# Optimization experiments

Hardware: AMD Instinct MI355X
Metric: run time of the kernel (lower is better)

Reference implementation:

```python
import jax, jax.numpy as jnp
import numpy as np

D = 512      # d_model
H = 8        # num_heads
HD = D // H  # head_dim = 64
NI = 3       # num_inputs


def setup_inputs() -> dict:
    key = jax.random.key(0)
    ks = jax.random.split(key, 20)
    b, n, ni = 4, 8192, 4096
    s = 0.02
    inp = {
        "x": jax.random.normal(ks[0], (b, n, D), jnp.float32),
        "emb0": jax.random.normal(ks[1], (b, ni, D), jnp.float32),
        "emb1": jax.random.normal(ks[2], (b, ni, D), jnp.float32),
        "emb2": jax.random.normal(ks[3], (b, ni, D), jnp.float32),
        "Wq": jax.random.normal(ks[4], (D, D), jnp.float32) * s,
        "bq": jnp.zeros((D,), jnp.float32),
        "Wk": jax.random.normal(ks[5], (NI, D, D), jnp.float32) * s,
        "bk": jnp.zeros((NI, D), jnp.float32),
        "Wv": jax.random.normal(ks[6], (NI, D, D), jnp.float32) * s,
        "bv": jnp.zeros((NI, D), jnp.float32),
        "Wo": jax.random.normal(ks[7], (D, D), jnp.float32) * s,
        "bo": jnp.zeros((D,), jnp.float32),
        "mask0": jax.random.randint(ks[8], (b, ni), 0, 2).astype(bool),
        "mask1": jax.random.randint(ks[9], (b, ni), 0, 2).astype(bool),
        "mask2": jax.random.randint(ks[10], (b, ni), 0, 2).astype(bool),
    }
    return inp


def _heads(t, b):
    # [b, n, D] -> [b, H, n, HD]
    return t.reshape(b, -1, H, HD).transpose(0, 2, 1, 3)


def reference(x, emb0, emb1, emb2, Wq, bq, Wk, bk, Wv, bv, Wo, bo, mask0, mask1, mask2):
    b, n, _ = x.shape
    q = jax.nn.softmax(_heads(x @ Wq.T + bq, b), axis=-1)  # [b,H,n,HD]
    out = q
    for i, (emb, mask) in enumerate(((emb0, mask0), (emb1, mask1), (emb2, mask2))):
        k = jax.nn.softmax(_heads(emb @ Wk[i].T + bk[i], b), axis=-1)  # [b,H,ni,HD]
        v = _heads(emb @ Wv[i].T + bv[i], b)                            # [b,H,ni,HD]
        k = jnp.where(mask[:, None, :, None], k, 0.0)
        k_sum = k.sum(axis=2, keepdims=True)                            # [b,H,1,HD]
        d_inv = 1.0 / jnp.sum(q * k_sum, axis=-1, keepdims=True)        # [b,H,n,1]
        kv = jnp.einsum('bhsd,bhse->bhde', k, v)                        # [b,H,HD,HD]
        out = out + jnp.einsum('bhnd,bhde->bhne', q, kv) * d_inv
    out = out.transpose(0, 2, 1, 3).reshape(b, n, D) / NI
    return out @ Wo.T + bo
```

## Files before the change

kernel.cpp:

```cpp
#include <hip/hip_runtime.h>

#define D_MODEL 512
#define NH 8
#define HD_ 64
#define NUM_I 3
#define B_ 4
#define NSEQ 8192
#define SSEQ 4096

typedef __attribute__((ext_vector_type(8))) short short8;
typedef __attribute__((ext_vector_type(4))) float floatx4;

static constexpr size_t Q_OFF    = 0;
static constexpr size_t KBUF_OFF = 8388608;
static constexpr size_t VBUF_OFF = 16777216;
static constexpr size_t EMBB_OFF = 25165824;
static constexpr size_t WB_OFF   = 29360128;
static constexpr size_t KV_OFF   = 30408704;
static constexpr size_t KS_OFF   = 30801920;
static constexpr size_t FLAG_OFF = 30808064;

__device__ __forceinline__ float bf2f(unsigned short u) {
    union { unsigned i; float f; } v; v.i = ((unsigned)u) << 16; return v.f;
}
__device__ __forceinline__ unsigned short f2bf(float f) {
    union { float f; unsigned i; } v; v.f = f;
    unsigned r = v.i + 0x7fffu + ((v.i >> 16) & 1u);
    return (unsigned short)(r >> 16);
}

__device__ __forceinline__ void gld16(const void* g, void* l) {
    __builtin_amdgcn_global_load_lds((const __attribute__((address_space(1))) void*)g,
                                     (__attribute__((address_space(3))) void*)l, 16, 0, 0);
}

__global__ void mask_mode_kernel(const int* __restrict__ m, int* __restrict__ flag)
{
    __shared__ int any;
    if (threadIdx.x == 0) any = 0;
    __syncthreads();
    const unsigned v = (unsigned)m[threadIdx.x];
    if (v > 1u) atomicOr(&any, 1);
    __syncthreads();
    if (threadIdx.x == 0) *flag = any;
}

__global__ __launch_bounds__(256)
void f2bf_kernel(const float* __restrict__ in, unsigned short* __restrict__ out, int n8)
{
    const int i = blockIdx.x * 256 + threadIdx.x;
    if (i >= n8) return;
    const float4 a = ((const float4*)in)[2*i];
    const float4 b = ((const float4*)in)[2*i + 1];
    short8 r;
    r[0] = (short)f2bf(a.x); r[1] = (short)f2bf(a.y);
    r[2] = (short)f2bf(a.z); r[3] = (short)f2bf(a.w);
    r[4] = (short)f2bf(b.x); r[5] = (short)f2bf(b.y);
    r[6] = (short)f2bf(b.z); r[7] = (short)f2bf(b.w);
    ((short8*)out)[i] = r;
}

template<int EPI, bool BF16OUT>
__global__ __launch_bounds__(256)
void proj_mfma(const unsigned short* __restrict__ A, const unsigned short* __restrict__ W,
               const float* __restrict__ bias, const int* __restrict__ mask,
               const int* __restrict__ maskmode, void* __restrict__ Cv)
{
    __shared__ short As[4096];
    __shared__ short Bs[4096];
    const int tid  = threadIdx.x;
    const int wid  = tid >> 6, lane = tid & 63;
    const int wm   = wid & 1,  wn   = wid >> 1;
    const int l15  = lane & 15, lq  = lane >> 4;
    const int m0   = blockIdx.x * 128;
    const int n0   = blockIdx.y * 128;

    floatx4 acc[4][4] = {};

    const int srow = tid & 127;
    const int sks  = tid >> 7;
    const unsigned short* Ag = A + (size_t)(m0 + srow) * D_MODEL + sks * 8;
    const unsigned short* Wg = W + (size_t)(n0 + srow) * D_MODEL + sks * 8;
    short* AsW = As + wid * 512;
    short* BsW = Bs + wid * 512;

    const int aoff = (lq * 128 + wm * 64 + l15) * 8;
    const int boff = (lq * 128 + wn * 64 + l15) * 8;

    for (int k0 = 0; k0 < D_MODEL; k0 += 32) {
        __syncthreads();
        gld16(Ag + k0,      AsW);
        gld16(Ag + k0 + 16, AsW + 2048);
        gld16(Wg + k0,      BsW);
        gld16(Wg + k0 + 16, BsW + 2048);
        __syncthreads();
        short8 af[4], bfv[4];
#pragma unroll
        for (int mt = 0; mt < 4; ++mt) af[mt]  = *(const short8*)&As[aoff + mt * 128];
#pragma unroll
        for (int nt = 0; nt < 4; ++nt) bfv[nt] = *(const short8*)&Bs[boff + nt * 128];
#pragma unroll
        for (int mt = 0; mt < 4; ++mt)
#pragma unroll
            for (int nt = 0; nt < 4; ++nt)
                acc[mt][nt] = __builtin_amdgcn_mfma_f32_16x16x32_bf16(af[mt], bfv[nt], acc[mt][nt], 0, 0, 0);
    }

    float bl[4];
#pragma unroll
    for (int nt = 0; nt < 4; ++nt) bl[nt] = bias[n0 + wn * 64 + nt * 16 + l15];
#pragma unroll
    for (int mt = 0; mt < 4; ++mt)
#pragma unroll
        for (int nt = 0; nt < 4; ++nt)
#pragma unroll
            for (int r = 0; r < 4; ++r) acc[mt][nt][r] += bl[nt];

    if (EPI >= 1) {
#pragma unroll
        for (int mt = 0; mt < 4; ++mt)
#pragma unroll
            for (int r = 0; r < 4; ++r) {
                float mx = fmaxf(fmaxf(acc[mt][0][r], acc[mt][1][r]),
                                 fmaxf(acc[mt][2][r], acc[mt][3][r]));
#pragma unroll
                for (int off = 1; off < 16; off <<= 1) mx = fmaxf(mx, __shfl_xor(mx, off));
                float s = 0.f;
#pragma unroll
                for (int nt = 0; nt < 4; ++nt) {
                    const float e = __expf(acc[mt][nt][r] - mx);
                    acc[mt][nt][r] = e; s += e;
                }
#pragma unroll
                for (int off = 1; off < 16; off <<= 1) s += __shfl_xor(s, off);
                const float inv = 1.f / s;
#pragma unroll
                for (int nt = 0; nt < 4; ++nt) acc[mt][nt][r] *= inv;
            }
    }
    if (EPI == 2) {
        const int bytemode = *maskmode;
#pragma unroll
        for (int mt = 0; mt < 4; ++mt)
#pragma unroll
            for (int r = 0; r < 4; ++r) {
                const int grow = m0 + wm * 64 + mt * 16 + lq * 4 + r;
                const bool keep = bytemode ? (((const unsigned char*)mask)[grow] != 0)
                                           : (mask[grow] != 0);
                if (!keep) {
#pragma unroll
                    for (int nt = 0; nt < 4; ++nt) acc[mt][nt][r] = 0.f;
                }
            }
    }

#pragma unroll
    for (int mt = 0; mt < 4; ++mt)
#pragma unroll
        for (int r = 0; r < 4; ++r) {
            const size_t row = m0 + wm * 64 + mt * 16 + lq * 4 + r;
#pragma unroll
            for (int nt = 0; nt < 4; ++nt) {
                const int col = n0 + wn * 64 + nt * 16 + l15;
                if (BF16OUT)
                    ((unsigned short*)Cv)[row * D_MODEL + col] = f2bf(acc[mt][nt][r]);
                else
                    ((float*)Cv)[row * D_MODEL + col] = acc[mt][nt][r];
            }
        }
}

__global__ __launch_bounds__(256)
void kv_accum_kernel(const float* __restrict__ K, const float* __restrict__ V,
                     float* __restrict__ kv, float* __restrict__ ksum, int i_idx)
{
    const int chunk = blockIdx.x;
    const int h = blockIdx.y;
    const int b = blockIdx.z;
    __shared__ __align__(16) float ks[32][68];
    __shared__ __align__(16) float vs[32][68];
    const int tid = threadIdx.x;
    const int tx = tid & 15, ty = tid >> 4;
    const int lrow = tid >> 4;
    const int lq = (tid & 15) << 2;
    float acc[4][4];
#pragma unroll
    for (int r = 0; r < 4; ++r)
#pragma unroll
        for (int c = 0; c < 4; ++c) acc[r][c] = 0.f;
    float ksloc = 0.f;
    const size_t base = (size_t)b * SSEQ * D_MODEL + h * HD_;

    for (int s0 = chunk*512; s0 < chunk*512 + 512; s0 += 32) {
        const float4 k0v = *(const float4*)&K[base + (size_t)(s0+lrow)    * D_MODEL + lq];
        const float4 k1v = *(const float4*)&K[base + (size_t)(s0+lrow+16) * D_MODEL + lq];
        const float4 v0v = *(const float4*)&V[base + (size_t)(s0+lrow)    * D_MODEL + lq];
        const float4 v1v = *(const float4*)&V[base + (size_t)(s0+lrow+16) * D_MODEL + lq];
        __syncthreads();
        *(float4*)&ks[lrow][lq]    = k0v;
        *(float4*)&ks[lrow+16][lq] = k1v;
        *(float4*)&vs[lrow][lq]    = v0v;
        *(float4*)&vs[lrow+16][lq] = v1v;
        __syncthreads();
#pragma unroll
        for (int s = 0; s < 32; ++s) {
            const float4 ka = *(const float4*)&ks[s][ty*4];
            const float4 vb = *(const float4*)&vs[s][tx*4];
            const float av[4] = {ka.x,ka.y,ka.z,ka.w};
            const float bv[4] = {vb.x,vb.y,vb.z,vb.w};
#pragma unroll
            for (int r = 0; r < 4; ++r)
#pragma unroll
                for (int c = 0; c < 4; ++c)
                    acc[r][c] = fmaf(av[r], bv[c], acc[r][c]);
        }
        if (tid < 64) {
#pragma unroll
            for (int s = 0; s < 32; ++s) ksloc += ks[s][tid];
        }
    }
    float* kvb = kv + ((size_t)((i_idx*B_ + b)*NH + h) << 12);
#pragma unroll
    for (int r = 0; r < 4; ++r)
#pragma unroll
        for (int c = 0; c < 4; ++c)
            atomicAdd(&kvb[(ty*4+r)*HD_ + tx*4+c], acc[r][c]);
    if (tid < 64)
        atomicAdd(&ksum[(size_t)((i_idx*B_ + b)*NH + h)*HD_ + tid], ksloc);
}

__global__ __launch_bounds__(256)
void combine_kernel(const unsigned short* __restrict__ Q, const float* __restrict__ kv,
                    const float* __restrict__ ksum, unsigned short* __restrict__ Qo)
{
    const int m0 = blockIdx.x * 128;
    const int h  = blockIdx.y;
    const int b  = m0 >> 13;
    __shared__ __align__(16) float Qt[64][128];
    __shared__ __align__(16) float Bs[64][68];
    __shared__ float sk[NUM_I][64];
    __shared__ float dinv[NUM_I][128];
    const int tid = threadIdx.x;
    const int tx = tid & 15, ty = tid >> 4;

#pragma unroll
    for (int it = 0; it < 4; ++it) {
        const int j = tid + it*256;
        const int row = j >> 3;
        const int c0  = (j & 7) << 3;
        const short8 g = *(const short8*)&Q[(size_t)(m0+row)*D_MODEL + h*HD_ + c0];
#pragma unroll
        for (int t = 0; t < 8; ++t) Qt[c0+t][row] = bf2f((unsigned short)g[t]);
    }
    if (tid < NUM_I*64) {
        const int i = tid >> 6, d = tid & 63;
        sk[i][d] = ksum[(size_t)((i*B_ + b)*NH + h)*HD_ + d];
    }
    __syncthreads();
    for (int idx = tid; idx < NUM_I*128; idx += 256) {
        const int i = idx >> 7, row = idx & 127;
        float dsum = 0.f;
#pragma unroll
        for (int dd = 0; dd < 64; ++dd) dsum += Qt[dd][row] * sk[i][dd];
        dinv[i][row] = 1.f / dsum;
    }

    float accO[8][4];
#pragma unroll
    for (int r = 0; r < 8; ++r)
#pragma unroll
        for (int c = 0; c < 4; ++c) accO[r][c] = 0.f;

    for (int i = 0; i < NUM_I; ++i) {
        const float* kvb = kv + ((size_t)((i*B_ + b)*NH + h) << 12);
        __syncthreads();
#pragma unroll
        for (int it = 0; it < 4; ++it) {
            const int j = tid + it*256;
            *(float4*)&Bs[j >> 4][(j & 15) << 2] = *(const float4*)&kvb[(size_t)j << 2];
        }
        __syncthreads();
        float part[8][4];
#pragma unroll
        for (int r = 0; r < 8; ++r)
#pragma unroll
            for (int c = 0; c < 4; ++c) part[r][c] = 0.f;
#pragma unroll
        for (int kk = 0; kk < 64; ++kk) {
            const float4 fa0 = *(const float4*)&Qt[kk][ty*8];
            const float4 fa1 = *(const float4*)&Qt[kk][ty*8+4];
            const float4 fb  = *(const float4*)&Bs[kk][tx*4];
            const float av[8] = {fa0.x,fa0.y,fa0.z,fa0.w,fa1.x,fa1.y,fa1.z,fa1.w};
            const float bv[4] = {fb.x,fb.y,fb.z,fb.w};
#pragma unroll
            for (int r = 0; r < 8; ++r)
#pragma unroll
                for (int c = 0; c < 4; ++c)
                    part[r][c] = fmaf(av[r], bv[c], part[r][c]);
        }
#pragma unroll
        for (int r = 0; r < 8; ++r) {
            const float dv = dinv[i][ty*8 + r];
#pragma unroll
            for (int c = 0; c < 4; ++c) accO[r][c] = fmaf(part[r][c], dv, accO[r][c]);
        }
    }
    const float inv3 = 1.f / 3.f;
#pragma unroll
    for (int r = 0; r < 8; ++r) {
        const int row = ty*8 + r;
        ushort4 o;
        o.x = f2bf((Qt[tx*4+0][row] + accO[r][0]) * inv3);
        o.y = f2bf((Qt[tx*4+1][row] + accO[r][1]) * inv3);
        o.z = f2bf((Qt[tx*4+2][row] + accO[r][2]) * inv3);
        o.w = f2bf((Qt[tx*4+3][row] + accO[r][3]) * inv3);
        *(ushort4*)&Qo[(size_t)(m0+row)*D_MODEL + h*HD_ + tx*4] = o;
    }
}

extern "C" void kernel_launch(void* const* d_in, const int* in_sizes, int n_in,
                              void* d_out, int out_size, void* d_ws, size_t ws_size,
                              hipStream_t stream)
{
    const float* x      = (const float*)d_in[0];
    const float* emb[3] = {(const float*)d_in[1], (const float*)d_in[2], (const float*)d_in[3]};
    const float* Wq = (const float*)d_in[4];
    const float* bq = (const float*)d_in[5];
    const float* Wk = (const float*)d_in[6];
    const float* bk = (const float*)d_in[7];
    const float* Wv = (const float*)d_in[8];
    const float* bv = (const float*)d_in[9];
    const float* Wo = (const float*)d_in[10];
    const float* bo = (const float*)d_in[11];
    const int* mask[3] = {(const int*)d_in[12], (const int*)d_in[13], (const int*)d_in[14]};
    float* out = (float*)d_out;

    float* ws = (float*)d_ws;
    unsigned short* qb   = (unsigned short*)(ws + Q_OFF);
    float*          kbuf = ws + KBUF_OFF;
    float*          vbuf = ws + VBUF_OFF;
    unsigned short* xb   = (unsigned short*)(ws + VBUF_OFF);
    unsigned short* embb = (unsigned short*)(ws + EMBB_OFF);
    unsigned short* wb   = (unsigned short*)(ws + WB_OFF);
    unsigned short* wqb  = wb;
    unsigned short* wkb  = wb + 262144;
    unsigned short* wvb  = wb + 1048576;
    unsigned short* wob  = wb + 1835008;
    unsigned short* q2b  = (unsigned short*)(ws + KBUF_OFF);
    float* kv   = ws + KV_OFF;
    float* ksum = ws + KS_OFF;
    int*   flag = (int*)(ws + FLAG_OFF);

    mask_mode_kernel<<<1, 256, 0, stream>>>(mask[0], flag);
    hipMemsetAsync(kv, 0, (size_t)(NUM_I*B_*NH*HD_*HD_ + NUM_I*B_*NH*HD_) * sizeof(float), stream);

    f2bf_kernel<<<8192, 256, 0, stream>>>(x,  xb,  2097152);
    f2bf_kernel<<<128,  256, 0, stream>>>(Wq, wqb, 32768);
    f2bf_kernel<<<384,  256, 0, stream>>>(Wk, wkb, 98304);
    f2bf_kernel<<<384,  256, 0, stream>>>(Wv, wvb, 98304);
    f2bf_kernel<<<128,  256, 0, stream>>>(Wo, wob, 32768);

    const dim3 gq(B_*NSEQ/128, D_MODEL/128);
    const dim3 gk(B_*SSEQ/128, D_MODEL/128);

    proj_mfma<1, true ><<<gq, 256, 0, stream>>>(xb, wqb, bq, nullptr, nullptr, qb);
    for (int i = 0; i < NUM_I; ++i) {
        f2bf_kernel<<<4096, 256, 0, stream>>>(emb[i], embb, 1048576);
        proj_mfma<2, false><<<gk, 256, 0, stream>>>(embb, wkb + (size_t)i*262144,
                                                    bk + (size_t)i*D_MODEL, mask[i], flag, kbuf);
        proj_mfma<0, false><<<gk, 256, 0, stream>>>(embb, wvb + (size_t)i*262144,
                                                    bv + (size_t)i*D_MODEL, nullptr, nullptr, vbuf);
        kv_accum_kernel<<<dim3(8, NH, B_), 256, 0, stream>>>(kbuf, vbuf, kv, ksum, i);
    }
    combine_kernel<<<dim3(B_*NSEQ/128, NH), 256, 0, stream>>>(qb, kv, ksum, q2b);
    proj_mfma<0, false><<<gq, 256, 0, stream>>>(q2b, wob, bo, nullptr, nullptr, out);
}
```

Baseline: 712.8 us.

## Move KV accumulation and combine to bf16 MFMA with transposed K/V layout

The K and V projections now write bf16 outputs transposed per head (head-dim rows by sequence), staged through shared memory. This lets a new MFMA-based kv-accumulation kernel read contiguous sequence chunks and compute the key sum with a ones-vector MFMA. The combine step also uses MFMA, reading a bf16 copy of the kv state. This removes the fp32 scalar FMA loops and halves K/V intermediate traffic. The cost is extra bf16 rounding of K, V and kv, plus a small conversion kernel.

```diff
diff --git a/kernel.cpp b/kernel.cpp
--- a/kernel.cpp
+++ b/kernel.cpp
@@ -12,13 +12,16 @@
 typedef __attribute__((ext_vector_type(4))) float floatx4;
 
 static constexpr size_t Q_OFF    = 0;
-static constexpr size_t KBUF_OFF = 8388608;
-static constexpr size_t VBUF_OFF = 16777216;
-static constexpr size_t EMBB_OFF = 25165824;
-static constexpr size_t WB_OFF   = 29360128;
-static constexpr size_t KV_OFF   = 30408704;
-static constexpr size_t KS_OFF   = 30801920;
-static constexpr size_t FLAG_OFF = 30808064;
+static constexpr size_t KT_OFF   = 8388608;
+static constexpr size_t VT_OFF   = 12582912;
+static constexpr size_t XB_OFF   = 8388608;
+static constexpr size_t Q2_OFF   = 8388608;
+static constexpr size_t EMBB_OFF = 16777216;
+static constexpr size_t WB_OFF   = 20971520;
+static constexpr size_t KV_OFF   = 22020096;
+static constexpr size_t KS_OFF   = 22413312;
+static constexpr size_t KVB_OFF  = 22419456;
+static constexpr size_t FLAG_OFF = 22616064;
 
 __device__ __forceinline__ float bf2f(unsigned short u) {
     union { unsigned i; float f; } v; v.i = ((unsigned)u) << 16; return v.f;
@@ -28,7 +31,6 @@
     unsigned r = v.i + 0x7fffu + ((v.i >> 16) & 1u);
     return (unsigned short)(r >> 16);
 }
-
 __device__ __forceinline__ void gld16(const void* g, void* l) {
     __builtin_amdgcn_global_load_lds((const __attribute__((address_space(1))) void*)g,
                                      (__attribute__((address_space(3))) void*)l, 16, 0, 0);
@@ -60,14 +62,15 @@
     ((short8*)out)[i] = r;
 }
 
-template<int EPI, bool BF16OUT>
+template<int EPI, int OUT>
 __global__ __launch_bounds__(256)
 void proj_mfma(const unsigned short* __restrict__ A, const unsigned short* __restrict__ W,
                const float* __restrict__ bias, const int* __restrict__ mask,
                const int* __restrict__ maskmode, void* __restrict__ Cv)
 {
-    __shared__ short As[4096];
-    __shared__ short Bs[4096];
+    __shared__ short smem[(OUT == 2) ? 18432 : 8192];
+    short* As = smem;
+    short* Bs = smem + 4096;
     const int tid  = threadIdx.x;
     const int wid  = tid >> 6, lane = tid & 63;
     const int wm   = wid & 1,  wn   = wid >> 1;
@@ -154,168 +157,193 @@
             }
     }
 
-#pragma unroll
-    for (int mt = 0; mt < 4; ++mt)
-#pragma unroll
-        for (int r = 0; r < 4; ++r) {
-            const size_t row = m0 + wm * 64 + mt * 16 + lq * 4 + r;
+    if (OUT == 2) {
+        __syncthreads();
+        short* tw = smem + wid * 4608;
+#pragma unroll
+        for (int mt = 0; mt < 4; ++mt)
 #pragma unroll
             for (int nt = 0; nt < 4; ++nt) {
-                const int col = n0 + wn * 64 + nt * 16 + l15;
-                if (BF16OUT)
-                    ((unsigned short*)Cv)[row * D_MODEL + col] = f2bf(acc[mt][nt][r]);
-                else
-                    ((float*)Cv)[row * D_MODEL + col] = acc[mt][nt][r];
-            }
+                ushort4 p;
+                p.x = f2bf(acc[mt][nt][0]); p.y = f2bf(acc[mt][nt][1]);
+                p.z = f2bf(acc[mt][nt][2]); p.w = f2bf(acc[mt][nt][3]);
+                *(ushort4*)&tw[(nt*16 + l15)*72 + mt*16 + lq*4] = p;
+            }
+        __syncthreads();
+        const int b_idx = m0 >> 12;
+        const int s_base = (m0 & 4095) + wm * 64;
+        const int h = (n0 >> 6) + wn;
+        unsigned short* outp = (unsigned short*)Cv +
+            ((size_t)(b_idx * NH + h) * 64 + lane) * SSEQ + s_base;
+        const short* src = &tw[lane * 72];
+#pragma unroll
+        for (int sc = 0; sc < 8; ++sc)
+            *(short8*)&outp[sc*8] = *(const short8*)&src[sc*8];
+    } else {
+#pragma unroll
+        for (int mt = 0; mt < 4; ++mt)
+#pragma unroll
+            for (int r = 0; r < 4; ++r) {
+                const size_t row = m0 + wm * 64 + mt * 16 + lq * 4 + r;
+#pragma unroll
+                for (int nt = 0; nt < 4; ++nt) {
+                    const int col = n0 + wn * 64 + nt * 16 + l15;
+                    if (OUT == 1)
+                        ((unsigned short*)Cv)[row * D_MODEL + col] = f2bf(acc[mt][nt][r]);
+                    else
+                        ((float*)Cv)[row * D_MODEL + col] = acc[mt][nt][r];
+                }
+            }
+    }
+}
+
+__global__ __launch_bounds__(256)
+void kv_accum_mfma(const unsigned short* __restrict__ kT, const unsigned short* __restrict__ vT,
+                   float* __restrict__ kv, float* __restrict__ ksum, int i_idx)
+{
+    const int chunk = blockIdx.x;
+    const int h = blockIdx.y, b = blockIdx.z;
+    __shared__ short As[2048];
+    __shared__ short Bs[2048];
+    const int tid = threadIdx.x;
+    const int wid = tid >> 6, lane = tid & 63;
+    const int wm  = wid & 1,  wn  = wid >> 1;
+    const int l15 = lane & 15, lq = lane >> 4;
+
+    const size_t base = (size_t)(b * NH + h) * 64 * SSEQ + chunk * 512;
+    const int srow = tid & 63, ssub = tid >> 6;
+    const unsigned short* Ag = vT + base + (size_t)srow * SSEQ + ssub * 8;
+    const unsigned short* Bg = kT + base + (size_t)srow * SSEQ + ssub * 8;
+    short* AsW = As + wid * 512;
+    short* BsW = Bs + wid * 512;
+
+    floatx4 acc[2][2] = {};
+    floatx4 ks[2] = {};
+    short8 ones;
+#pragma unroll
+    for (int j = 0; j < 8; ++j) ones[j] = (short)0x3F80;
+
+    const int aoff = (wm*32 + l15)*8;
+    const int boff = (wn*32 + l15)*8;
+
+    for (int k0 = 0; k0 < 512; k0 += 32) {
+        __syncthreads();
+        gld16(Ag + k0, AsW);
+        gld16(Bg + k0, BsW);
+        __syncthreads();
+        short8 af[2], bfr[2];
+#pragma unroll
+        for (int mt = 0; mt < 2; ++mt) af[mt]  = *(const short8*)&As[lq*512 + aoff + mt*128];
+#pragma unroll
+        for (int nt = 0; nt < 2; ++nt) bfr[nt] = *(const short8*)&Bs[lq*512 + boff + nt*128];
+#pragma unroll
+        for (int mt = 0; mt < 2; ++mt)
+#pragma unroll
+            for (int nt = 0; nt < 2; ++nt)
+                acc[mt][nt] = __builtin_amdgcn_mfma_f32_16x16x32_bf16(af[mt], bfr[nt], acc[mt][nt], 0, 0, 0);
+        if (wm == 0) {
+#pragma unroll
+            for (int nt = 0; nt < 2; ++nt)
+                ks[nt] = __builtin_amdgcn_mfma_f32_16x16x32_bf16(ones, bfr[nt], ks[nt], 0, 0, 0);
         }
+    }
+    float* kvb = kv + (size_t)((i_idx*B_ + b)*NH + h) * 4096;
+#pragma unroll
+    for (int mt = 0; mt < 2; ++mt)
+#pragma unroll
+        for (int nt = 0; nt < 2; ++nt)
+#pragma unroll
+            for (int r = 0; r < 4; ++r) {
+                const int e = wm*32 + mt*16 + lq*4 + r;
+                const int d = wn*32 + nt*16 + l15;
+                atomicAdd(&kvb[e*64 + d], acc[mt][nt][r]);
+            }
+    if (wm == 0 && lq == 0) {
+        float* ksb = ksum + (size_t)((i_idx*B_ + b)*NH + h) * 64;
+#pragma unroll
+        for (int nt = 0; nt < 2; ++nt)
+            atomicAdd(&ksb[wn*32 + nt*16 + l15], ks[nt][0]);
+    }
 }
 
 __global__ __launch_bounds__(256)
-void kv_accum_kernel(const float* __restrict__ K, const float* __restrict__ V,
-                     float* __restrict__ kv, float* __restrict__ ksum, int i_idx)
-{
-    const int chunk = blockIdx.x;
-    const int h = blockIdx.y;
-    const int b = blockIdx.z;
-    __shared__ __align__(16) float ks[32][68];
-    __shared__ __align__(16) float vs[32][68];
-    const int tid = threadIdx.x;
-    const int tx = tid & 15, ty = tid >> 4;
-    const int lrow = tid >> 4;
-    const int lq = (tid & 15) << 2;
-    float acc[4][4];
-#pragma unroll
-    for (int r = 0; r < 4; ++r)
-#pragma unroll
-        for (int c = 0; c < 4; ++c) acc[r][c] = 0.f;
-    float ksloc = 0.f;
-    const size_t base = (size_t)b * SSEQ * D_MODEL + h * HD_;
-
-    for (int s0 = chunk*512; s0 < chunk*512 + 512; s0 += 32) {
-        const float4 k0v = *(const float4*)&K[base + (size_t)(s0+lrow)    * D_MODEL + lq];
-        const float4 k1v = *(const float4*)&K[base + (size_t)(s0+lrow+16) * D_MODEL + lq];
-        const float4 v0v = *(const float4*)&V[base + (size_t)(s0+lrow)    * D_MODEL + lq];
-        const float4 v1v = *(const float4*)&V[base + (size_t)(s0+lrow+16) * D_MODEL + lq];
-        __syncthreads();
-        *(float4*)&ks[lrow][lq]    = k0v;
-        *(float4*)&ks[lrow+16][lq] = k1v;
-        *(float4*)&vs[lrow][lq]    = v0v;
-        *(float4*)&vs[lrow+16][lq] = v1v;
-        __syncthreads();
-#pragma unroll
-        for (int s = 0; s < 32; ++s) {
-            const float4 ka = *(const float4*)&ks[s][ty*4];
-            const float4 vb = *(const float4*)&vs[s][tx*4];
-            const float av[4] = {ka.x,ka.y,ka.z,ka.w};
-            const float bv[4] = {vb.x,vb.y,vb.z,vb.w};
-#pragma unroll
-            for (int r = 0; r < 4; ++r)
-#pragma unroll
-                for (int c = 0; c < 4; ++c)
-                    acc[r][c] = fmaf(av[r], bv[c], acc[r][c]);
-        }
-        if (tid < 64) {
-#pragma unroll
-            for (int s = 0; s < 32; ++s) ksloc += ks[s][tid];
-        }
-    }
-    float* kvb = kv + ((size_t)((i_idx*B_ + b)*NH + h) << 12);
-#pragma unroll
-    for (int r = 0; r < 4; ++r)
-#pragma unroll
-        for (int c = 0; c < 4; ++c)
-            atomicAdd(&kvb[(ty*4+r)*HD_ + tx*4+c], acc[r][c]);
-    if (tid < 64)
-        atomicAdd(&ksum[(size_t)((i_idx*B_ + b)*NH + h)*HD_ + tid], ksloc);
-}
-
-__global__ __launch_bounds__(256)
-void combine_kernel(const unsigned short* __restrict__ Q, const float* __restrict__ kv,
-                    const float* __restrict__ ksum, unsigned short* __restrict__ Qo)
+void combine_mfma(const unsigned short* __restrict__ Q, const unsigned short* __restrict__ kvT,
+                  const float* __restrict__ ksum, unsigned short* __restrict__ Qo)
 {
     const int m0 = blockIdx.x * 128;
     const int h  = blockIdx.y;
     const int b  = m0 >> 13;
-    __shared__ __align__(16) float Qt[64][128];
-    __shared__ __align__(16) float Bs[64][68];
-    __shared__ float sk[NUM_I][64];
+    __shared__ short qs[8192];
+    __shared__ float skl[NUM_I][64];
     __shared__ float dinv[NUM_I][128];
     const int tid = threadIdx.x;
-    const int tx = tid & 15, ty = tid >> 4;
-
-#pragma unroll
-    for (int it = 0; it < 4; ++it) {
-        const int j = tid + it*256;
-        const int row = j >> 3;
-        const int c0  = (j & 7) << 3;
-        const short8 g = *(const short8*)&Q[(size_t)(m0+row)*D_MODEL + h*HD_ + c0];
-#pragma unroll
-        for (int t = 0; t < 8; ++t) Qt[c0+t][row] = bf2f((unsigned short)g[t]);
-    }
-    if (tid < NUM_I*64) {
+    const int wid = tid >> 6, lane = tid & 63;
+    const int l15 = lane & 15, lq = lane >> 4;
+
+    const unsigned short* Qbase = Q + (size_t)m0 * D_MODEL + h * 64;
+#pragma unroll
+    for (int j = 0; j < 4; ++j) {
+        const int g = tid + j * 256;
+        const int row = g & 127, c = g >> 7;
+        gld16(Qbase + (size_t)row * D_MODEL + c * 8, qs + (size_t)(wid*64 + j*256) * 8);
+    }
+    if (tid < NUM_I * 64) {
         const int i = tid >> 6, d = tid & 63;
-        sk[i][d] = ksum[(size_t)((i*B_ + b)*NH + h)*HD_ + d];
+        skl[i][d] = ksum[(size_t)((i*B_ + b)*NH + h) * 64 + d];
     }
     __syncthreads();
-    for (int idx = tid; idx < NUM_I*128; idx += 256) {
-        const int i = idx >> 7, row = idx & 127;
-        float dsum = 0.f;
-#pragma unroll
-        for (int dd = 0; dd < 64; ++dd) dsum += Qt[dd][row] * sk[i][dd];
-        dinv[i][row] = 1.f / dsum;
-    }
-
-    float accO[8][4];
-#pragma unroll
-    for (int r = 0; r < 8; ++r)
-#pragma unroll
-        for (int c = 0; c < 4; ++c) accO[r][c] = 0.f;
-
+    for (int it = tid; it < NUM_I * 128; it += 256) {
+        const int i = it >> 7, row = it & 127;
+        float s = 0.f;
+#pragma unroll
+        for (int d = 0; d < 64; ++d)
+            s += bf2f((unsigned short)qs[(d >> 3)*1024 + row*8 + (d & 7)]) * skl[i][d];
+        dinv[i][row] = 1.f / s;
+    }
+    __syncthreads();
+
+    short8 af[2][2];
+#pragma unroll
+    for (int mt = 0; mt < 2; ++mt)
+#pragma unroll
+        for (int ks = 0; ks < 2; ++ks)
+            af[mt][ks] = *(const short8*)&qs[(ks*4 + lq)*1024 + (wid*32 + mt*16 + l15)*8];
+
+    floatx4 accO[2][4] = {};
     for (int i = 0; i < NUM_I; ++i) {
-        const float* kvb = kv + ((size_t)((i*B_ + b)*NH + h) << 12);
-        __syncthreads();
-#pragma unroll
-        for (int it = 0; it < 4; ++it) {
-            const int j = tid + it*256;
-            *(float4*)&Bs[j >> 4][(j & 15) << 2] = *(const float4*)&kvb[(size_t)j << 2];
-        }
-        __syncthreads();
-        float part[8][4];
-#pragma unroll
-        for (int r = 0; r < 8; ++r)
-#pragma unroll
-            for (int c = 0; c < 4; ++c) part[r][c] = 0.f;
-#pragma unroll
-        for (int kk = 0; kk < 64; ++kk) {
-            const float4 fa0 = *(const float4*)&Qt[kk][ty*8];
-            const float4 fa1 = *(const float4*)&Qt[kk][ty*8+4];
-            const float4 fb  = *(const float4*)&Bs[kk][tx*4];
-            const float av[8] = {fa0.x,fa0.y,fa0.z,fa0.w,fa1.x,fa1.y,fa1.z,fa1.w};
-            const float bv[4] = {fb.x,fb.y,fb.z,fb.w};
-#pragma unroll
-            for (int r = 0; r < 8; ++r)
-#pragma unroll
-                for (int c = 0; c < 4; ++c)
-                    part[r][c] = fmaf(av[r], bv[c], part[r][c]);
-        }
-#pragma unroll
-        for (int r = 0; r < 8; ++r) {
-            const float dv = dinv[i][ty*8 + r];
-#pragma unroll
-            for (int c = 0; c < 4; ++c) accO[r][c] = fmaf(part[r][c], dv, accO[r][c]);
-        }
+        const unsigned short* kvb = kvT + (size_t)((i*B_ + b)*NH + h) * 4096;
+        short8 bfr[4][2];
+#pragma unroll
+        for (int nt = 0; nt < 4; ++nt)
+#pragma unroll
+            for (int ks = 0; ks < 2; ++ks)
+                bfr[nt][ks] = *(const short8*)&kvb[(nt*16 + l15)*64 + ks*32 + lq*8];
+#pragma unroll
+        for (int mt = 0; mt < 2; ++mt)
+#pragma unroll
+            for (int nt = 0; nt < 4; ++nt) {
+                floatx4 p = {};
+                p = __builtin_amdgcn_mfma_f32_16x16x32_bf16(af[mt][0], bfr[nt][0], p, 0, 0, 0);
+                p = __builtin_amdgcn_mfma_f32_16x16x32_bf16(af[mt][1], bfr[nt][1], p, 0, 0, 0);
+#pragma unroll
+                for (int r = 0; r < 4; ++r) {
+                    const int row = wid*32 + mt*16 + lq*4 + r;
+                    accO[mt][nt][r] += p[r] * dinv[i][row];
+                }
+            }
     }
     const float inv3 = 1.f / 3.f;
 #pragma unroll
-    for (int r = 0; r < 8; ++r) {
-        const int row = ty*8 + r;
-        ushort4 o;
-        o.x = f2bf((Qt[tx*4+0][row] + accO[r][0]) * inv3);
-        o.y = f2bf((Qt[tx*4+1][row] + accO[r][1]) * inv3);
-        o.z = f2bf((Qt[tx*4+2][row] + accO[r][2]) * inv3);
-        o.w = f2bf((Qt[tx*4+3][row] + accO[r][3]) * inv3);
-        *(ushort4*)&Qo[(size_t)(m0+row)*D_MODEL + h*HD_ + tx*4] = o;
-    }
+    for (int mt = 0; mt < 2; ++mt)
+#pragma unroll
+        for (int nt = 0; nt < 4; ++nt)
+#pragma unroll
+            for (int r = 0; r < 4; ++r) {
+                const int row = wid*32 + mt*16 + lq*4 + r;
+                const int col = nt*16 + l15;
+                const float qv = bf2f((unsigned short)qs[(col >> 3)*1024 + row*8 + (col & 7)]);
+                Qo[(size_t)(m0 + row) * D_MODEL + h*64 + col] = f2bf((qv + accO[mt][nt][r]) * inv3);
+            }
 }
 
 extern "C" void kernel_launch(void* const* d_in, const int* in_sizes, int n_in,
@@ -337,18 +365,19 @@
 
     float* ws = (float*)d_ws;
     unsigned short* qb   = (unsigned short*)(ws + Q_OFF);
-    float*          kbuf = ws + KBUF_OFF;
-    float*          vbuf = ws + VBUF_OFF;
-    unsigned short* xb   = (unsigned short*)(ws + VBUF_OFF);
+    unsigned short* kT   = (unsigned short*)(ws + KT_OFF);
+    unsigned short* vT   = (unsigned short*)(ws + VT_OFF);
+    unsigned short* xb   = (unsigned short*)(ws + XB_OFF);
+    unsigned short* q2b  = (unsigned short*)(ws + Q2_OFF);
     unsigned short* embb = (unsigned short*)(ws + EMBB_OFF);
     unsigned short* wb   = (unsigned short*)(ws + WB_OFF);
     unsigned short* wqb  = wb;
     unsigned short* wkb  = wb + 262144;
     unsigned short* wvb  = wb + 1048576;
     unsigned short* wob  = wb + 1835008;
-    unsigned short* q2b  = (unsigned short*)(ws + KBUF_OFF);
     float* kv   = ws + KV_OFF;
     float* ksum = ws + KS_OFF;
+    unsigned short* kvb16 = (unsigned short*)(ws + KVB_OFF);
     int*   flag = (int*)(ws + FLAG_OFF);
 
     mask_mode_kernel<<<1, 256, 0, stream>>>(mask[0], flag);
@@ -363,15 +392,16 @@
     const dim3 gq(B_*NSEQ/128, D_MODEL/128);
     const dim3 gk(B_*SSEQ/128, D_MODEL/128);
 
-    proj_mfma<1, true ><<<gq, 256, 0, stream>>>(xb, wqb, bq, nullptr, nullptr, qb);
+    proj_mfma<1, 1><<<gq, 256, 0, stream>>>(xb, wqb, bq, nullptr, nullptr, qb);
     for (int i = 0; i < NUM_I; ++i) {
         f2bf_kernel<<<4096, 256, 0, stream>>>(emb[i], embb, 1048576);
-        proj_mfma<2, false><<<gk, 256, 0, stream>>>(embb, wkb + (size_t)i*262144,
-                                                    bk + (size_t)i*D_MODEL, mask[i], flag, kbuf);
-        proj_mfma<0, false><<<gk, 256, 0, stream>>>(embb, wvb + (size_t)i*262144,
-                                                    bv + (size_t)i*D_MODEL, nullptr, nullptr, vbuf);
-        kv_accum_kernel<<<dim3(8, NH, B_), 256, 0, stream>>>(kbuf, vbuf, kv, ksum, i);
-    }
-    combine_kernel<<<dim3(B_*NSEQ/128, NH), 256, 0, stream>>>(qb, kv, ksum, q2b);
-    proj_mfma<0, false><<<gq, 256, 0, stream>>>(q2b, wob, bo, nullptr, nullptr, out);
-}
+        proj_mfma<2, 2><<<gk, 256, 0, stream>>>(embb, wkb + (size_t)i*262144,
+                                                bk + (size_t)i*D_MODEL, mask[i], flag, kT);
+        proj_mfma<0, 2><<<gk, 256, 0, stream>>>(embb, wvb + (size_t)i*262144,
+                                                bv + (size_t)i*D_MODEL, nullptr, nullptr, vT);
+        kv_accum_mfma<<<dim3(8, NH, B_), 256, 0, stream>>>(kT, vT, kv, ksum, i);
+    }
+    f2bf_kernel<<<192, 256, 0, stream>>>(kv, kvb16, 49152);
+    combine_mfma<<<dim3(B_*NSEQ/128, NH), 256, 0, stream>>>(qb, kvb16, ksum, q2b);
+    proj_mfma<0, 0><<<gq, 256, 0, stream>>>(q2b, wob, bo, nullptr, nullptr, out);
+}
```

After: 581.3 us. 1.23x faster.
